# Performance work log

Hardware: AMD Instinct MI355X
Metric: run time of the kernel (lower is better)

The kernel has to match this reference:

```python
import jax, jax.numpy as jnp
import numpy as np

G = 60   # rotation group size
K = 13   # SO3 neighbors per group element


def data_process(x, nei):
    # x: [B, C, 60] -> gather neighbors -> [B, C, 60, 13]
    b, c = x.shape[0], x.shape[1]
    return x[:, :, nei].reshape(b, c, G, K)


def comb_conv(x4, W, b):
    # x4: [B, C, 60, 13], W: [O, C, 13] (Conv2d kernel (1,13) squeezed) -> [B, O, 60]
    return jnp.einsum('bcgk,ock->bog', x4, W) + b[None, :, None]


def bn_relu(x, gamma, beta):
    # eval-mode BatchNorm2d folded to per-channel affine, then ReLU
    return jax.nn.relu(x * gamma[None, :, None] + beta[None, :, None])


def group_feat_net(feats, nei, W_in, b_in, W1, b1, g1, be1, W2, b2, g2, be2, Wo, bo, go, beo):
    # Conv_in: plain conv, no BN/ReLU
    d = comb_conv(data_process(feats, nei), W_in, b_in)              # [B,256,60]
    # Residual_Comb_Conv(256,512,256)
    fc = bn_relu(comb_conv(data_process(d, nei), W1, b1), g1, be1)   # [B,512,60]
    fc = bn_relu(comb_conv(data_process(fc, nei), W2, b2), g2, be2)  # [B,256,60]
    d = d + fc
    # Conv_out = Comb_Conv(256,32)
    d = bn_relu(comb_conv(data_process(d, nei), Wo, bo), go, beo)    # [B,32,60]
    eqv = d + feats
    inv = jnp.mean(eqv, axis=-1)                                     # [B,32]
    eqv = eqv / jnp.maximum(jnp.linalg.norm(eqv, axis=1, keepdims=True), 1e-4)
    inv = inv / jnp.maximum(jnp.linalg.norm(inv, axis=1, keepdims=True), 1e-4)
    return inv, eqv


def des2dr(des1, des2, permu):
    # des1, des2: [B,32,60]; permu: [3600] -> gather -> [B,32,60,60]
    b, f = des1.shape[0], des1.shape[1]
    d1p = des1[:, :, permu].reshape(b, f, G, G)
    cor = jnp.einsum('bfag,bfg->ba', d1p, des2)                      # [B,60]
    return jnp.argmax(cor, axis=1)


def setup_inputs() -> dict:
    key = jax.random.key(0)
    ks = jax.random.split(key, 16)
    B = 256
    inp = {
        'feats0': jax.random.normal(ks[0], (B, 32, G), dtype=jnp.float32),
        'feats1': jax.random.normal(ks[1], (B, 32, G), dtype=jnp.float32),
        'true_idx': jax.random.randint(ks[2], (B,), 0, G, dtype=jnp.int32),
        'nei_idx': jax.random.randint(ks[3], (G * K,), 0, G, dtype=jnp.int32),
        'permu_idx': jax.random.randint(ks[4], (G * G,), 0, G, dtype=jnp.int32),
        'W_in': jax.random.normal(ks[5], (256, 32, K), dtype=jnp.float32) * 0.05,
        'b_in': jnp.zeros((256,), dtype=jnp.float32),
        'W1': jax.random.normal(ks[6], (512, 256, K), dtype=jnp.float32) * 0.02,
        'b1': jnp.zeros((512,), dtype=jnp.float32),
        'g1': jnp.ones((512,), dtype=jnp.float32),
        'be1': jnp.zeros((512,), dtype=jnp.float32),
        'W2': jax.random.normal(ks[7], (256, 512, K), dtype=jnp.float32) * 0.02,
        'b2': jnp.zeros((256,), dtype=jnp.float32),
        'g2': jnp.ones((256,), dtype=jnp.float32),
        'be2': jnp.zeros((256,), dtype=jnp.float32),
        'Wo': jax.random.normal(ks[8], (32, 256, K), dtype=jnp.float32) * 0.02,
        'bo': jnp.zeros((32,), dtype=jnp.float32),
        'go': jnp.ones((32,), dtype=jnp.float32),
        'beo': jnp.zeros((32,), dtype=jnp.float32),
    }
    return inp


def reference(feats0, feats1, true_idx, nei_idx, permu_idx,
              W_in, b_in, W1, b1, g1, be1, W2, b2, g2, be2, Wo, bo, go, beo):
    params = (W_in, b_in, W1, b1, g1, be1, W2, b2, g2, be2, Wo, bo, go, beo)
    inv0, eqv0 = group_feat_net(feats0, nei_idx, *params)
    inv1, eqv1 = group_feat_net(feats1, nei_idx, *params)
    pre_idxs = des2dr(eqv0, eqv1, permu_idx)
    ability = jnp.mean((pre_idxs == true_idx).astype(jnp.float32))
    return (feats0, feats1, eqv0, eqv1, inv0, inv1, ability, true_idx, pre_idxs)
```

## Files before the change

kernel.cpp:

```cpp
#include <hip/hip_runtime.h>

#define G60 60
#define KN 13

typedef unsigned int u32;
typedef unsigned short u16;
typedef short short8 __attribute__((ext_vector_type(8)));
typedef float f32x4 __attribute__((ext_vector_type(4)));
typedef float f32x16 __attribute__((ext_vector_type(16)));
typedef u32 u32x4 __attribute__((ext_vector_type(4)));

template <int I> struct Ic { static constexpr int v = I; };
template <int I, int N, typename F>
__device__ __forceinline__ void sfor(F&& f) {
    if constexpr (I < N) { f(Ic<I>{}); sfor<I + 1, N>(f); }
}

__device__ __forceinline__ u32 f32_to_packed(float v) {
    u32 u = __float_as_uint(v);
    u32 hi = (u + 0x7FFFu + ((u >> 16) & 1u)) >> 16;
    float vhi = __uint_as_float(hi << 16);
    float lof = v - vhi;
    u32 ul = __float_as_uint(lof);
    u32 lo = (ul + 0x7FFFu + ((ul >> 16) & 1u)) >> 16;
    return (hi << 16) | lo;
}
__device__ __forceinline__ float packed_f32(u32 w) {
    return __uint_as_float(w & 0xFFFF0000u) + __uint_as_float(w << 16);
}

__device__ __forceinline__ void pack_one(const float* __restrict__ W,
                                         u16* __restrict__ Whi, u16* __restrict__ Wlo,
                                         int C, int O, int CT, int id) {
    int j = id & 7;
    int lane = (id >> 3) & 63;
    int fid = id >> 9;
    int NTt = O >> 5;
    int nt = fid % NTt;
    int t = fid / NTt;
    int SUBS = CT >> 4;
    int sub = t % SUBS;
    int kk = (t / SUBS) % KN;
    int ct = t / (KN * SUBS);
    int q = lane >> 5, n = lane & 31;
    int o = nt * 32 + n;
    int c = ct * CT + sub * 16 + q * 8 + j;
    u32 pw = f32_to_packed(W[((size_t)o * C + c) * KN + kk]);
    Whi[id] = (u16)(pw >> 16);
    Wlo[id] = (u16)(pw & 0xFFFFu);
}

__global__ void __launch_bounds__(256) pack_all_kern(
    const float* W_in, u16* Whi_in, u16* Wlo_in,
    const float* W1, u16* Whi_1, u16* Wlo_1,
    const float* W2, u16* Whi_2, u16* Wlo_2,
    const float* Wo, u16* Whi_o, u16* Wlo_o) {
    const int T0 = KN * 32 * 256;
    const int T1 = T0 + KN * 256 * 512;
    const int T2 = T1 + KN * 512 * 256;
    const int T3 = T2 + KN * 256 * 32;
    int id = blockIdx.x * 256 + threadIdx.x;
    if (id < T0) pack_one(W_in, Whi_in, Wlo_in, 32, 256, 32, id);
    else if (id < T1) pack_one(W1, Whi_1, Wlo_1, 256, 512, 64, id - T0);
    else if (id < T2) pack_one(W2, Whi_2, Wlo_2, 512, 256, 64, id - T1);
    else if (id < T3) pack_one(Wo, Whi_o, Wlo_o, 256, 32, 64, id - T2);
}

template <int CT, int WM, int WN, int SRC, bool BNR, bool OUTF32>
__global__ void __launch_bounds__(256, 2) mconv10(
    const u32* __restrict__ Xp, const float* __restrict__ Xf,
    const float* __restrict__ pIn,
    const float* __restrict__ bnb, const float* __restrict__ bng,
    const float* __restrict__ bnB,
    const u32* __restrict__ resid,
    const u16* __restrict__ Whi, const u16* __restrict__ Wlo,
    const float* __restrict__ bias, const float* __restrict__ gamma,
    const float* __restrict__ beta,
    const int* __restrict__ nei,
    u32* __restrict__ outp, float* __restrict__ outf,
    int C, int O, int tpz) {
    constexpr int SUBS = CT >> 4;
    constexpr int S = KN * SUBS;
    constexpr int NG = S / 2;
    constexpr int STRIDE = CT + 8;
    constexpr int PLSZ = G60 * STRIDE;
    constexpr int NMG = 4 / WM;
    constexpr int NRO = (WM == 4) ? 2 : WM;
    __shared__ u16 Xs[4 * PLSZ];
    const int tid = threadIdx.x;
    const int lane = tid & 63;
    const int wv = tid >> 6;
    const int mg = wv % NMG;
    const int ng = wv / NMG;
    const int q = lane >> 5;
    const int m = lane & 31;
    const int bp = blockIdx.x;
    const int NTt = O >> 5;
    const int nt0 = (int)blockIdx.y * (WM * WN) + ng * WN;
    const int ct0 = (int)blockIdx.z * tpz;
    const size_t PLi = (size_t)256 * C * G60;
    float* outfz = OUTF32 ? (outf + (size_t)blockIdx.z * ((size_t)256 * O * G60)) : nullptr;

    int rowoff[NRO][KN];
#pragma unroll
    for (int jj = 0; jj < NRO; ++jj) {
        int mts, base;
        if (WM == 4) { mts = jj; base = 0; }
        else {
            int s = mg * WM + jj;
            mts = s & 1;
            base = (s >> 1) * 2 * PLSZ;
        }
        int g = mts * 32 + m;
        int gl = (g < G60) ? g : 0;
#pragma unroll
        for (int kk = 0; kk < KN; ++kk)
            rowoff[jj][kk] = nei[gl * KN + kk] * STRIDE + base;
    }

    f32x16 acc[WM][WN];
#pragma unroll
    for (int j = 0; j < WM; ++j)
#pragma unroll
        for (int nt = 0; nt < WN; ++nt) acc[j][nt] = (f32x16)(0.f);

    short8 Bh[2][2][WN], Bl[2][2][WN];

    for (int ct = ct0; ct < ct0 + tpz; ++ct) {
        const size_t fbase = ((size_t)(ct * S) * NTt + nt0) * 512 + (size_t)lane * 8;

        __syncthreads();
        constexpr int PAIRS = (CT / 2) * G60;
        for (int i = tid; i < 2 * PAIRS; i += 256) {
            int sb = (i >= PAIRS) ? 1 : 0;
            int r = i - sb * PAIRS;
            int ccp = (r * 17477) >> 20;
            int g = r - ccp * G60;
            int cc = ccp * 2;
            size_t cg0 = ((size_t)(bp * 2 + sb) * C + (size_t)ct * CT + cc) * G60 + g;
            u32 w0, w1;
            if (SRC == 0) {
                w0 = Xp[cg0]; w1 = Xp[cg0 + G60];
            } else if (SRC == 1) {
                w0 = f32_to_packed(Xf[cg0]); w1 = f32_to_packed(Xf[cg0 + G60]);
            } else {
                int c0 = ct * CT + cc;
                float v0 = pIn[cg0] + pIn[PLi + cg0];
                float v1 = pIn[cg0 + G60] + pIn[PLi + cg0 + G60];
                v0 = fmaxf((v0 + bnb[c0]) * bng[c0] + bnB[c0], 0.f) + packed_f32(resid[cg0]);
                v1 = fmaxf((v1 + bnb[c0 + 1]) * bng[c0 + 1] + bnB[c0 + 1], 0.f) + packed_f32(resid[cg0 + G60]);
                w0 = f32_to_packed(v0); w1 = f32_to_packed(v1);
            }
            int rb = sb * 2 * PLSZ + g * STRIDE + cc;
            *(u32*)(Xs + rb) = (w0 >> 16) | (w1 & 0xFFFF0000u);
            *(u32*)(Xs + rb + PLSZ) = (w0 & 0xFFFFu) | (w1 << 16);
        }

        sfor<0, 2>([&](auto uc) {
            constexpr int u = decltype(uc)::v;
            sfor<0, WN>([&](auto nc) {
                constexpr int nt = decltype(nc)::v;
                const size_t fb = fbase + ((size_t)u * NTt + nt) * 512;
                Bh[0][u][nt] = *reinterpret_cast<const short8*>(Whi + fb);
                Bl[0][u][nt] = *reinterpret_cast<const short8*>(Wlo + fb);
            });
        });
        __syncthreads();

        sfor<0, NG>([&](auto gc) {
            constexpr int g = decltype(gc)::v;
            constexpr int pb = g & 1;
            if constexpr (g + 1 < NG) {
                constexpr int pn = (g + 1) & 1;
                sfor<0, 2>([&](auto uc) {
                    constexpr int u = decltype(uc)::v;
                    constexpr int s = 2 * (g + 1) + u;
                    sfor<0, WN>([&](auto nc) {
                        constexpr int nt = decltype(nc)::v;
                        const size_t fb = fbase + ((size_t)s * NTt + nt) * 512;
                        Bh[pn][u][nt] = *reinterpret_cast<const short8*>(Whi + fb);
                        Bl[pn][u][nt] = *reinterpret_cast<const short8*>(Wlo + fb);
                    });
                });
            }
            short8 Ah[2][WM], Al[2][WM];
            sfor<0, 2>([&](auto uc) {
                constexpr int u = decltype(uc)::v;
                constexpr int s = 2 * g + u;
                constexpr int kk = s / SUBS;
                constexpr int sub = s - kk * SUBS;
                sfor<0, WM>([&](auto jc) {
                    constexpr int j = decltype(jc)::v;
                    int off;
                    if constexpr (WM == 4)
                        off = rowoff[j & 1][kk] + (j >> 1) * 2 * PLSZ + sub * 16 + q * 8;
                    else
                        off = rowoff[j][kk] + sub * 16 + q * 8;
                    Ah[u][j] = *reinterpret_cast<const short8*>(Xs + off);
                    Al[u][j] = *reinterpret_cast<const short8*>(Xs + off + PLSZ);
                });
            });
            sfor<0, 2>([&](auto uc) {
                constexpr int u = decltype(uc)::v;
                sfor<0, WN>([&](auto nc) {
                    constexpr int nt = decltype(nc)::v;
                    sfor<0, WM>([&](auto jc) {
                        constexpr int j = decltype(jc)::v;
                        acc[j][nt] = __builtin_amdgcn_mfma_f32_32x32x16_bf16(
                            Ah[u][j], Bh[pb][u][nt], acc[j][nt], 0, 0, 0);
                    });
                });
                sfor<0, WN>([&](auto nc) {
                    constexpr int nt = decltype(nc)::v;
                    sfor<0, WM>([&](auto jc) {
                        constexpr int j = decltype(jc)::v;
                        acc[j][nt] = __builtin_amdgcn_mfma_f32_32x32x16_bf16(
                            Ah[u][j], Bl[pb][u][nt], acc[j][nt], 0, 0, 0);
                    });
                });
                sfor<0, WN>([&](auto nc) {
                    constexpr int nt = decltype(nc)::v;
                    sfor<0, WM>([&](auto jc) {
                        constexpr int j = decltype(jc)::v;
                        acc[j][nt] = __builtin_amdgcn_mfma_f32_32x32x16_bf16(
                            Al[u][j], Bh[pb][u][nt], acc[j][nt], 0, 0, 0);
                    });
                });
            });
        });
    }

#pragma unroll
    for (int j = 0; j < WM; ++j) {
        const int s = mg * WM + j;
        const int bbs = s >> 1, mts = s & 1;
        const int b = bp * 2 + bbs;
#pragma unroll
        for (int nt = 0; nt < WN; ++nt) {
            const int o = (nt0 + nt) * 32 + m;
            float bi = 0.f, ga = 1.f, be = 0.f;
            if (!OUTF32) { bi = bias[o]; if (BNR) { ga = gamma[o]; be = beta[o]; } }
#pragma unroll
            for (int grp = 0; grp < 4; ++grp) {
                const int g0 = mts * 32 + grp * 8 + q * 4;
                if (g0 < G60) {
                    size_t oi = ((size_t)b * O + o) * G60 + g0;
                    if (OUTF32) {
                        f32x4 v;
#pragma unroll
                        for (int rr = 0; rr < 4; ++rr) v[rr] = acc[j][nt][grp * 4 + rr];
                        *reinterpret_cast<f32x4*>(outfz + oi) = v;
                    } else {
                        u32x4 pv;
#pragma unroll
                        for (int rr = 0; rr < 4; ++rr) {
                            float v = acc[j][nt][grp * 4 + rr] + bi;
                            if (BNR) v = fmaxf(v * ga + be, 0.f);
                            pv[rr] = f32_to_packed(v);
                        }
                        *reinterpret_cast<u32x4*>(outp + oi) = pv;
                    }
                }
            }
        }
    }
}

__global__ void __launch_bounds__(64) finalize_kern(
    const float* __restrict__ pout,
    const float* __restrict__ feats,
    const float* __restrict__ bo, const float* __restrict__ go,
    const float* __restrict__ beo,
    float* __restrict__ out_feats,
    float* __restrict__ out_eqv,
    float* __restrict__ out_inv) {
    const int b = blockIdx.x;
    const size_t PB = (size_t)256 * 32 * G60;
    __shared__ float E[32 * G60];
    __shared__ float gnorm[G60];
    __shared__ float inv_pre[32];
    __shared__ float inv_nrm;
    const int tid = threadIdx.x;

    for (int i = tid; i < 32 * G60; i += 64) {
        int f = i / G60;
        size_t idx = (size_t)b * 1920 + i;
        float ft = feats[idx];
        out_feats[idx] = ft;
        float s = pout[idx] + pout[PB + idx] + pout[2 * PB + idx] + pout[3 * PB + idx];
        float v = fmaxf((s + bo[f]) * go[f] + beo[f], 0.f);
        E[i] = v + ft;
    }
    __syncthreads();
    if (tid < G60) {
        float s = 0.f;
        for (int f = 0; f < 32; ++f) { float v = E[f * G60 + tid]; s += v * v; }
        gnorm[tid] = fmaxf(sqrtf(s), 1e-4f);
    }
    if (tid < 32) {
        float s = 0.f;
        for (int g = 0; g < G60; ++g) s += E[tid * G60 + g];
        inv_pre[tid] = s / 60.f;
    }
    __syncthreads();
    if (tid == 0) {
        float s = 0.f;
        for (int f = 0; f < 32; ++f) s += inv_pre[f] * inv_pre[f];
        inv_nrm = fmaxf(sqrtf(s), 1e-4f);
    }
    __syncthreads();
    for (int i = tid; i < 1920; i += 64) {
        int g = i % G60;
        out_eqv[(size_t)b * 1920 + i] = E[i] / gnorm[g];
    }
    if (tid < 32) out_inv[b * 32 + tid] = inv_pre[tid] / inv_nrm;
}

__global__ void __launch_bounds__(256) des2dr_kern(
    const float* __restrict__ e0f, const float* __restrict__ e1f,
    const int* __restrict__ permu, int* __restrict__ pre_int,
    float* __restrict__ out_pre) {
    const int b = blockIdx.x;
    __shared__ float X0[32 * G60];
    __shared__ float X1[32 * G60];
    __shared__ float pc[256];
    __shared__ float cor[64];
    const int tid = threadIdx.x;
    for (int i = tid; i < 1920; i += 256) {
        X0[i] = e0f[(size_t)b * 1920 + i];
        X1[i] = e1f[(size_t)b * 1920 + i];
    }
    __syncthreads();
    const int a = tid >> 2, fc = tid & 3;
    float s = 0.f;
    if (a < G60) {
        for (int g = 0; g < G60; ++g) {
            int p = permu[a * G60 + g];
#pragma unroll
            for (int f = fc * 8; f < fc * 8 + 8; ++f) s += X0[f * G60 + p] * X1[f * G60 + g];
        }
    }
    pc[tid] = s;
    __syncthreads();
    if (tid < 64) cor[tid] = pc[4 * tid] + pc[4 * tid + 1] + pc[4 * tid + 2] + pc[4 * tid + 3];
    __syncthreads();
    if (tid == 0) {
        float best = cor[0];
        int bi = 0;
        for (int a2 = 1; a2 < G60; ++a2)
            if (cor[a2] > best) { best = cor[a2]; bi = a2; }
        pre_int[b] = bi;
        out_pre[b] = (float)bi;
    }
}

__global__ void __launch_bounds__(256) ability_kern(
    const int* __restrict__ pre_int, const int* __restrict__ true_idx,
    float* __restrict__ out_ability, float* __restrict__ out_true) {
    __shared__ int cnt[256];
    const int t = threadIdx.x;
    cnt[t] = (pre_int[t] == true_idx[t]) ? 1 : 0;
    out_true[t] = (float)true_idx[t];
    __syncthreads();
    for (int s = 128; s > 0; s >>= 1) {
        if (t < s) cnt[t] += cnt[t + s];
        __syncthreads();
    }
    if (t == 0) out_ability[0] = (float)cnt[0] / 256.0f;
}

extern "C" void kernel_launch(void* const* d_in, const int* in_sizes, int n_in,
                              void* d_out, int out_size, void* d_ws, size_t ws_size,
                              hipStream_t stream) {
    const float* feats0 = (const float*)d_in[0];
    const float* feats1 = (const float*)d_in[1];
    const int* true_idx = (const int*)d_in[2];
    const int* nei = (const int*)d_in[3];
    const int* permu = (const int*)d_in[4];
    const float* W_in = (const float*)d_in[5];
    const float* b_in = (const float*)d_in[6];
    const float* W1 = (const float*)d_in[7];
    const float* b1 = (const float*)d_in[8];
    const float* g1 = (const float*)d_in[9];
    const float* be1 = (const float*)d_in[10];
    const float* W2 = (const float*)d_in[11];
    const float* b2 = (const float*)d_in[12];
    const float* g2 = (const float*)d_in[13];
    const float* be2 = (const float*)d_in[14];
    const float* Wo = (const float*)d_in[15];
    const float* bo = (const float*)d_in[16];
    const float* go = (const float*)d_in[17];
    const float* beo = (const float*)d_in[18];

    float* out = (float*)d_out;
    const size_t SZF = (size_t)256 * 32 * G60;
    float* out_f0 = out;
    float* out_f1 = out + SZF;
    float* out_e0 = out + 2 * SZF;
    float* out_e1 = out + 3 * SZF;
    float* out_i0 = out + 4 * SZF;
    float* out_i1 = out_i0 + 256 * 32;
    float* out_ab = out_i1 + 256 * 32;
    float* out_tr = out_ab + 1;
    float* out_pr = out_tr + 256;

    char* p = (char*)d_ws;
    auto alloc = [&](size_t bytes) { char* r = p; p += (bytes + 255) & ~(size_t)255; return r; };
    const size_t NW_IN = (size_t)KN * 32 * 256;
    const size_t NW_1 = (size_t)KN * 256 * 512;
    const size_t NW_2 = (size_t)KN * 512 * 256;
    const size_t NW_O = (size_t)KN * 256 * 32;
    u16* Whi_in = (u16*)alloc(NW_IN * 2); u16* Wlo_in = (u16*)alloc(NW_IN * 2);
    u16* Whi_1 = (u16*)alloc(NW_1 * 2);   u16* Wlo_1 = (u16*)alloc(NW_1 * 2);
    u16* Whi_2 = (u16*)alloc(NW_2 * 2);   u16* Wlo_2 = (u16*)alloc(NW_2 * 2);
    u16* Whi_o = (u16*)alloc(NW_O * 2);   u16* Wlo_o = (u16*)alloc(NW_O * 2);
    u32* dbuf = (u32*)alloc((size_t)256 * 256 * G60 * 4);
    u32* fcbuf = (u32*)alloc((size_t)256 * 512 * G60 * 4);
    float* p2 = (float*)alloc((size_t)2 * 256 * 256 * G60 * 4);
    float* pout = (float*)alloc((size_t)4 * SZF * 4);
    int* pre_int = (int*)alloc(256 * 4);

    {
        int total = KN * (32 * 256 + 256 * 512 + 512 * 256 + 256 * 32);
        pack_all_kern<<<dim3((total + 255) / 256), dim3(256), 0, stream>>>(
            W_in, Whi_in, Wlo_in, W1, Whi_1, Wlo_1, W2, Whi_2, Wlo_2, Wo, Whi_o, Wlo_o);
    }

    for (int net = 0; net < 2; ++net) {
        const float* feats = net ? feats1 : feats0;
        float* of = net ? out_f1 : out_f0;
        float* oe = net ? out_e1 : out_e0;
        float* oi = net ? out_i1 : out_i0;

        mconv10<32, 2, 1, 1, false, false><<<dim3(128, 4, 1), dim3(256), 0, stream>>>(
            nullptr, feats, nullptr, nullptr, nullptr, nullptr, nullptr,
            Whi_in, Wlo_in, b_in, nullptr, nullptr, nei, dbuf, nullptr, 32, 256, 1);
        mconv10<64, 4, 1, 0, true, false><<<dim3(128, 4, 1), dim3(256), 0, stream>>>(
            dbuf, nullptr, nullptr, nullptr, nullptr, nullptr, nullptr,
            Whi_1, Wlo_1, b1, g1, be1, nei, fcbuf, nullptr, 256, 512, 4);
        mconv10<64, 4, 1, 0, false, true><<<dim3(128, 2, 2), dim3(256), 0, stream>>>(
            fcbuf, nullptr, nullptr, nullptr, nullptr, nullptr, nullptr,
            Whi_2, Wlo_2, nullptr, nullptr, nullptr, nei, nullptr, p2, 512, 256, 4);
        mconv10<64, 1, 1, 2, false, true><<<dim3(128, 1, 4), dim3(256), 0, stream>>>(
            nullptr, nullptr, p2, b2, g2, be2, dbuf,
            Whi_o, Wlo_o, nullptr, nullptr, nullptr, nei, nullptr, pout, 256, 32, 1);
        finalize_kern<<<dim3(256), dim3(64), 0, stream>>>(pout, feats, bo, go, beo, of, oe, oi);
    }

    des2dr_kern<<<dim3(256), dim3(256), 0, stream>>>(out_e0, out_e1, permu, pre_int, out_pr);
    ability_kern<<<dim3(1), dim3(256), 0, stream>>>(pre_int, true_idx, out_ab, out_tr);

    (void)in_sizes; (void)n_in; (void)out_size; (void)ws_size;
}
```

Before: 774.0 us.

## Batch both feature networks into single launches over 512 samples

Processes feats0 and feats1 together as one batch of 512 in each conv and finalize kernel, which doubles the grid size and halves the number of launches. Per-batch pointer selection and a batch-base offset are added to the conv and finalize kernels. The merged path needs a larger workspace and falls back to the old per-network loop when ws_size is too small. The intent is to cut launch overhead and improve GPU occupancy, since 128-block grids underfill the chip.

```diff
diff --git a/kernel.cpp b/kernel.cpp
--- a/kernel.cpp
+++ b/kernel.cpp
@@ -67,8 +67,9 @@
 }
 
 template <int CT, int WM, int WN, int SRC, bool BNR, bool OUTF32>
-__global__ void __launch_bounds__(256, 2) mconv10(
-    const u32* __restrict__ Xp, const float* __restrict__ Xf,
+__global__ void __launch_bounds__(256, 2) mconv11(
+    const u32* __restrict__ Xp, const float* __restrict__ Xf0,
+    const float* __restrict__ Xf1,
     const float* __restrict__ pIn,
     const float* __restrict__ bnb, const float* __restrict__ bng,
     const float* __restrict__ bnB,
@@ -78,7 +79,7 @@
     const float* __restrict__ beta,
     const int* __restrict__ nei,
     u32* __restrict__ outp, float* __restrict__ outf,
-    int C, int O, int tpz) {
+    int C, int O, int tpz, int bbase, int NBb) {
     constexpr int SUBS = CT >> 4;
     constexpr int S = KN * SUBS;
     constexpr int NG = S / 2;
@@ -94,12 +95,12 @@
     const int ng = wv / NMG;
     const int q = lane >> 5;
     const int m = lane & 31;
-    const int bp = blockIdx.x;
+    const int bp = (int)blockIdx.x + (bbase >> 1);
     const int NTt = O >> 5;
     const int nt0 = (int)blockIdx.y * (WM * WN) + ng * WN;
     const int ct0 = (int)blockIdx.z * tpz;
-    const size_t PLi = (size_t)256 * C * G60;
-    float* outfz = OUTF32 ? (outf + (size_t)blockIdx.z * ((size_t)256 * O * G60)) : nullptr;
+    const size_t PLi = (size_t)NBb * C * G60;
+    float* outfz = OUTF32 ? (outf + (size_t)blockIdx.z * ((size_t)NBb * O * G60)) : nullptr;
 
     int rowoff[NRO][KN];
 #pragma unroll
@@ -137,13 +138,18 @@
             int ccp = (r * 17477) >> 20;
             int g = r - ccp * G60;
             int cc = ccp * 2;
-            size_t cg0 = ((size_t)(bp * 2 + sb) * C + (size_t)ct * CT + cc) * G60 + g;
+            const int bg = bp * 2 + sb;
+            const int bloc = bg - bbase;
             u32 w0, w1;
             if (SRC == 0) {
+                size_t cg0 = ((size_t)bloc * C + (size_t)ct * CT + cc) * G60 + g;
                 w0 = Xp[cg0]; w1 = Xp[cg0 + G60];
             } else if (SRC == 1) {
+                const float* Xf = (bg >= 256) ? Xf1 : Xf0;
+                size_t cg0 = ((size_t)(bg & 255) * C + (size_t)ct * CT + cc) * G60 + g;
                 w0 = f32_to_packed(Xf[cg0]); w1 = f32_to_packed(Xf[cg0 + G60]);
             } else {
+                size_t cg0 = ((size_t)bloc * C + (size_t)ct * CT + cc) * G60 + g;
                 int c0 = ct * CT + cc;
                 float v0 = pIn[cg0] + pIn[PLi + cg0];
                 float v1 = pIn[cg0 + G60] + pIn[PLi + cg0 + G60];
@@ -234,7 +240,7 @@
     for (int j = 0; j < WM; ++j) {
         const int s = mg * WM + j;
         const int bbs = s >> 1, mts = s & 1;
-        const int b = bp * 2 + bbs;
+        const int bloc = bp * 2 + bbs - bbase;
 #pragma unroll
         for (int nt = 0; nt < WN; ++nt) {
             const int o = (nt0 + nt) * 32 + m;
@@ -244,7 +250,7 @@
             for (int grp = 0; grp < 4; ++grp) {
                 const int g0 = mts * 32 + grp * 8 + q * 4;
                 if (g0 < G60) {
-                    size_t oi = ((size_t)b * O + o) * G60 + g0;
+                    size_t oi = ((size_t)bloc * O + o) * G60 + g0;
                     if (OUTF32) {
                         f32x4 v;
 #pragma unroll
@@ -268,14 +274,22 @@
 
 __global__ void __launch_bounds__(64) finalize_kern(
     const float* __restrict__ pout,
-    const float* __restrict__ feats,
+    const float* __restrict__ feats0, const float* __restrict__ feats1,
     const float* __restrict__ bo, const float* __restrict__ go,
     const float* __restrict__ beo,
-    float* __restrict__ out_feats,
-    float* __restrict__ out_eqv,
-    float* __restrict__ out_inv) {
-    const int b = blockIdx.x;
-    const size_t PB = (size_t)256 * 32 * G60;
+    float* __restrict__ of0, float* __restrict__ of1,
+    float* __restrict__ oe0, float* __restrict__ oe1,
+    float* __restrict__ oi0, float* __restrict__ oi1,
+    int bbase, int NBb) {
+    const int bloc = blockIdx.x;
+    const int bg = bloc + bbase;
+    const int net = bg >> 8;
+    const int bl = bg & 255;
+    const float* feats = net ? feats1 : feats0;
+    float* out_feats = net ? of1 : of0;
+    float* out_eqv = net ? oe1 : oe0;
+    float* out_inv = net ? oi1 : oi0;
+    const size_t PB = (size_t)NBb * 32 * G60;
     __shared__ float E[32 * G60];
     __shared__ float gnorm[G60];
     __shared__ float inv_pre[32];
@@ -284,9 +298,10 @@
 
     for (int i = tid; i < 32 * G60; i += 64) {
         int f = i / G60;
-        size_t idx = (size_t)b * 1920 + i;
-        float ft = feats[idx];
-        out_feats[idx] = ft;
+        size_t idx = (size_t)bloc * 1920 + i;
+        size_t idf = (size_t)bl * 1920 + i;
+        float ft = feats[idf];
+        out_feats[idf] = ft;
         float s = pout[idx] + pout[PB + idx] + pout[2 * PB + idx] + pout[3 * PB + idx];
         float v = fmaxf((s + bo[f]) * go[f] + beo[f], 0.f);
         E[i] = v + ft;
@@ -311,9 +326,9 @@
     __syncthreads();
     for (int i = tid; i < 1920; i += 64) {
         int g = i % G60;
-        out_eqv[(size_t)b * 1920 + i] = E[i] / gnorm[g];
-    }
-    if (tid < 32) out_inv[b * 32 + tid] = inv_pre[tid] / inv_nrm;
+        out_eqv[(size_t)bl * 1920 + i] = E[i] / gnorm[g];
+    }
+    if (tid < 32) out_inv[bl * 32 + tid] = inv_pre[tid] / inv_nrm;
 }
 
 __global__ void __launch_bounds__(256) des2dr_kern(
@@ -414,11 +429,9 @@
     u16* Whi_1 = (u16*)alloc(NW_1 * 2);   u16* Wlo_1 = (u16*)alloc(NW_1 * 2);
     u16* Whi_2 = (u16*)alloc(NW_2 * 2);   u16* Wlo_2 = (u16*)alloc(NW_2 * 2);
     u16* Whi_o = (u16*)alloc(NW_O * 2);   u16* Wlo_o = (u16*)alloc(NW_O * 2);
-    u32* dbuf = (u32*)alloc((size_t)256 * 256 * G60 * 4);
-    u32* fcbuf = (u32*)alloc((size_t)256 * 512 * G60 * 4);
-    float* p2 = (float*)alloc((size_t)2 * 256 * 256 * G60 * 4);
-    float* pout = (float*)alloc((size_t)4 * SZF * 4);
-    int* pre_int = (int*)alloc(256 * 4);
+
+    const size_t MERGED_NEED = 173000000;
+    const bool merged = ws_size >= MERGED_NEED;
 
     {
         int total = KN * (32 * 256 + 256 * 512 + 512 * 256 + 256 * 32);
@@ -426,29 +439,72 @@
             W_in, Whi_in, Wlo_in, W1, Whi_1, Wlo_1, W2, Whi_2, Wlo_2, Wo, Whi_o, Wlo_o);
     }
 
-    for (int net = 0; net < 2; ++net) {
-        const float* feats = net ? feats1 : feats0;
-        float* of = net ? out_f1 : out_f0;
-        float* oe = net ? out_e1 : out_e0;
-        float* oi = net ? out_i1 : out_i0;
-
-        mconv10<32, 2, 1, 1, false, false><<<dim3(128, 4, 1), dim3(256), 0, stream>>>(
-            nullptr, feats, nullptr, nullptr, nullptr, nullptr, nullptr,
-            Whi_in, Wlo_in, b_in, nullptr, nullptr, nei, dbuf, nullptr, 32, 256, 1);
-        mconv10<64, 4, 1, 0, true, false><<<dim3(128, 4, 1), dim3(256), 0, stream>>>(
-            dbuf, nullptr, nullptr, nullptr, nullptr, nullptr, nullptr,
-            Whi_1, Wlo_1, b1, g1, be1, nei, fcbuf, nullptr, 256, 512, 4);
-        mconv10<64, 4, 1, 0, false, true><<<dim3(128, 2, 2), dim3(256), 0, stream>>>(
-            fcbuf, nullptr, nullptr, nullptr, nullptr, nullptr, nullptr,
-            Whi_2, Wlo_2, nullptr, nullptr, nullptr, nei, nullptr, p2, 512, 256, 4);
-        mconv10<64, 1, 1, 2, false, true><<<dim3(128, 1, 4), dim3(256), 0, stream>>>(
-            nullptr, nullptr, p2, b2, g2, be2, dbuf,
-            Whi_o, Wlo_o, nullptr, nullptr, nullptr, nei, nullptr, pout, 256, 32, 1);
-        finalize_kern<<<dim3(256), dim3(64), 0, stream>>>(pout, feats, bo, go, beo, of, oe, oi);
-    }
-
-    des2dr_kern<<<dim3(256), dim3(256), 0, stream>>>(out_e0, out_e1, permu, pre_int, out_pr);
-    ability_kern<<<dim3(1), dim3(256), 0, stream>>>(pre_int, true_idx, out_ab, out_tr);
+    if (merged) {
+        u32* dbuf = (u32*)alloc((size_t)512 * 256 * G60 * 4);
+        u32* fcbuf = (u32*)alloc((size_t)512 * 512 * G60 * 4);
+        float* p2 = (float*)alloc((size_t)2 * 512 * 256 * G60 * 4);
+        float* pout = (float*)fcbuf;
+        int* pre_int = (int*)alloc(512 * 4);
+
+        mconv11<32, 2, 1, 1, false, false><<<dim3(256, 4, 1), dim3(256), 0, stream>>>(
+            nullptr, feats0, feats1, nullptr, nullptr, nullptr, nullptr, nullptr,
+            Whi_in, Wlo_in, b_in, nullptr, nullptr, nei, dbuf, nullptr,
+            32, 256, 1, 0, 512);
+        mconv11<64, 4, 1, 0, true, false><<<dim3(256, 4, 1), dim3(256), 0, stream>>>(
+            dbuf, nullptr, nullptr, nullptr, nullptr, nullptr, nullptr, nullptr,
+            Whi_1, Wlo_1, b1, g1, be1, nei, fcbuf, nullptr,
+            256, 512, 4, 0, 512);
+        mconv11<64, 4, 1, 0, false, true><<<dim3(256, 2, 2), dim3(256), 0, stream>>>(
+            fcbuf, nullptr, nullptr, nullptr, nullptr, nullptr, nullptr, nullptr,
+            Whi_2, Wlo_2, nullptr, nullptr, nullptr, nei, nullptr, p2,
+            512, 256, 4, 0, 512);
+        mconv11<64, 1, 1, 2, false, true><<<dim3(256, 1, 4), dim3(256), 0, stream>>>(
+            nullptr, nullptr, nullptr, p2, b2, g2, be2, dbuf,
+            Whi_o, Wlo_o, nullptr, nullptr, nullptr, nei, nullptr, pout,
+            256, 32, 1, 0, 512);
+        finalize_kern<<<dim3(512), dim3(64), 0, stream>>>(
+            pout, feats0, feats1, bo, go, beo,
+            out_f0, out_f1, out_e0, out_e1, out_i0, out_i1, 0, 512);
+    } else {
+        u32* dbuf = (u32*)alloc((size_t)256 * 256 * G60 * 4);
+        u32* fcbuf = (u32*)alloc((size_t)256 * 512 * G60 * 4);
+        float* p2 = (float*)alloc((size_t)2 * 256 * 256 * G60 * 4);
+        float* pout = (float*)alloc((size_t)4 * SZF * 4);
+        int* pre_int0 = (int*)alloc(256 * 4);
+
+        for (int net = 0; net < 2; ++net) {
+            const int bb = net * 256;
+            mconv11<32, 2, 1, 1, false, false><<<dim3(128, 4, 1), dim3(256), 0, stream>>>(
+                nullptr, feats0, feats1, nullptr, nullptr, nullptr, nullptr, nullptr,
+                Whi_in, Wlo_in, b_in, nullptr, nullptr, nei, dbuf, nullptr,
+                32, 256, 1, bb, 256);
+            mconv11<64, 4, 1, 0, true, false><<<dim3(128, 4, 1), dim3(256), 0, stream>>>(
+                dbuf, nullptr, nullptr, nullptr, nullptr, nullptr, nullptr, nullptr,
+                Whi_1, Wlo_1, b1, g1, be1, nei, fcbuf, nullptr,
+                256, 512, 4, bb, 256);
+            mconv11<64, 4, 1, 0, false, true><<<dim3(128, 2, 2), dim3(256), 0, stream>>>(
+                fcbuf, nullptr, nullptr, nullptr, nullptr, nullptr, nullptr, nullptr,
+                Whi_2, Wlo_2, nullptr, nullptr, nullptr, nei, nullptr, p2,
+                512, 256, 4, bb, 256);
+            mconv11<64, 1, 1, 2, false, true><<<dim3(128, 1, 4), dim3(256), 0, stream>>>(
+                nullptr, nullptr, nullptr, p2, b2, g2, be2, dbuf,
+                Whi_o, Wlo_o, nullptr, nullptr, nullptr, nei, nullptr, pout,
+                256, 32, 1, bb, 256);
+            finalize_kern<<<dim3(256), dim3(64), 0, stream>>>(
+                pout, feats0, feats1, bo, go, beo,
+                out_f0, out_f1, out_e0, out_e1, out_i0, out_i1, bb, 256);
+        }
+        des2dr_kern<<<dim3(256), dim3(256), 0, stream>>>(out_e0, out_e1, permu, pre_int0, out_pr);
+        ability_kern<<<dim3(1), dim3(256), 0, stream>>>(pre_int0, true_idx, out_ab, out_tr);
+        (void)in_sizes; (void)n_in; (void)out_size;
+        return;
+    }
+
+    {
+        int* pre_int = (int*)alloc(256 * 4);
+        des2dr_kern<<<dim3(256), dim3(256), 0, stream>>>(out_e0, out_e1, permu, pre_int, out_pr);
+        ability_kern<<<dim3(1), dim3(256), 0, stream>>>(pre_int, true_idx, out_ab, out_tr);
+    }
 
     (void)in_sizes; (void)n_in; (void)out_size; (void)ws_size;
 }
```

After: 720.9 us. -6.9%, faster.
